# Optimization experiments

Measured on AMD Instinct MI355X. Metric: run time of the kernel, lower is better.

The kernel has to match this reference:

```python
import jax, jax.numpy as jnp
import numpy as np

N = 10000      # nodes per QA graph
E = 128000     # edges per QA graph
A = 5          # answers (multiple choice)
D = 300        # glove embedding dim
H = 8          # heads layer 1
C1 = 64        # per-head out channels layer 1 (concat -> 512)
HID = 512
NEG_SLOPE = 0.2
EPS = 1e-16


def gat_layer(x, edge_index, W, a_src, a_dst, bias, concat):
    # x: [N, Din]; edge_index: [2, E]; W: [Din, H*C]; a_src/a_dst: [H, C]
    Hh, C = a_src.shape
    h = (x @ W).reshape(N, Hh, C)                      # transformed node feats
    alpha_src = (h * a_src[None]).sum(-1)              # [N, H]
    alpha_dst = (h * a_dst[None]).sum(-1)              # [N, H]
    src, dst = edge_index[0], edge_index[1]
    e = jax.nn.leaky_relu(alpha_src[src] + alpha_dst[dst], NEG_SLOPE)  # [E, H]
    # edge softmax grouped by destination node
    m = jax.ops.segment_max(e, dst, num_segments=N)    # [N, H]
    ex = jnp.exp(e - m[dst])
    denom = jax.ops.segment_sum(ex, dst, num_segments=N)
    alpha = ex / (denom[dst] + EPS)                    # [E, H]
    msg = alpha[:, :, None] * h[src]                   # [E, H, C]
    out = jax.ops.segment_sum(msg, dst, num_segments=N)  # [N, H, C]
    out = out.reshape(N, Hh * C) if concat else out.mean(axis=1)
    return out + bias, alpha


def setup_inputs() -> dict:
    key = jax.random.key(0)
    ks = jax.random.split(key, 10)
    s = 0.05
    return {
        "x": jax.random.normal(ks[0], (A, N, D), jnp.float32),
        "edge_index": jax.random.randint(ks[1], (A, 2, E), 0, N, dtype=jnp.int32),
        "W1": jax.random.normal(ks[2], (D, H * C1), jnp.float32) * s,
        "att_src1": jax.random.normal(ks[3], (H, C1), jnp.float32) * s,
        "att_dst1": jax.random.normal(ks[4], (H, C1), jnp.float32) * s,
        "bias1": jnp.zeros((H * C1,), jnp.float32),
        "W2": jax.random.normal(ks[5], (HID, 1), jnp.float32) * s,
        "att_src2": jax.random.normal(ks[6], (1, 1), jnp.float32) * s,
        "att_dst2": jax.random.normal(ks[7], (1, 1), jnp.float32) * s,
        "bias2": jnp.zeros((1,), jnp.float32),
    }


def reference(x, edge_index, W1, att_src1, att_dst1, bias1, W2, att_src2, att_dst2, bias2):
    def per_answer(xa, ei):
        h1, _ = gat_layer(xa, ei, W1, att_src1, att_dst1, bias1, concat=True)
        h1 = jax.nn.relu(h1)
        h2, alpha = gat_layer(h1, ei, W2, att_src2, att_dst2, bias2, concat=False)
        proba = h2.mean()                                  # scalar (x.mean(dim=0))
        # aggregate_attention: attention[dst] += edge_weight (edge_additive)
        att = jax.ops.segment_sum(alpha[:, 0], ei[1], num_segments=N)
        return proba, att

    proba_vec, atts = jax.vmap(per_answer)(x, edge_index)  # [A], [A, N]
    sel = atts[jnp.argmax(proba_vec)]                      # attentions[argmax]
    return proba_vec, sel
```

## Files before the change

### kernel.cpp

```cpp
#include <hip/hip_runtime.h>
#include <hip/hip_bf16.h>
#include <math.h>

#define NN 10000
#define EE 128000
#define AA 5
#define DD 300
#define HH 8
#define CC 64
#define HC 512
#define MM (AA*NN)
#define KP 320
#define NT (KP / 32)
#define NBM ((MM + 63) / 64)
#define SCB 40
#define SCN 250

typedef __attribute__((ext_vector_type(8))) _Float16 f16x8;
typedef __attribute__((ext_vector_type(4))) float f32x4;
typedef __attribute__((ext_vector_type(2))) float f32x2;
typedef unsigned short ushort;
typedef unsigned char uchar;

__device__ __forceinline__ ushort f2bf(float f) {
    unsigned u = __float_as_uint(f);
    unsigned r = u + 0x7fffu + ((u >> 16) & 1u);
    return (ushort)(r >> 16);
}
__device__ __forceinline__ float bf2f(ushort h) {
    return __uint_as_float(((unsigned)h) << 16);
}
__device__ __forceinline__ float leaky_exp(float v) {
    v = v > 0.f ? v : 0.2f * v;
    return __expf(v);
}


__global__ void zero_cnt(int* cnt) {
    int i = blockIdx.x * 256 + threadIdx.x;
    if (i < AA * NN) cnt[i] = 0;
}

__global__ void count_edges(const int* __restrict__ ei, int* __restrict__ cnt) {
    int a = blockIdx.y;
    int e = blockIdx.x * 256 + threadIdx.x;
    if (e < EE) {
        int dst = ei[(size_t)a * 2 * EE + EE + e];
        atomicAdd(&cnt[a * NN + dst], 1);
    }
}


__global__ __launch_bounds__(256) void scan_bsum(const int* __restrict__ cnt,
                                                 int* __restrict__ bsum) {
    int a = blockIdx.y, b = blockIdx.x;
    int l = threadIdx.x;
    int v = (l < SCN) ? cnt[a * NN + b * SCN + l] : 0;
    #pragma unroll
    for (int o = 1; o < 64; o <<= 1) v += __shfl_xor(v, o);
    __shared__ int red[4];
    if ((l & 63) == 0) red[l >> 6] = v;
    __syncthreads();
    if (l == 0) bsum[a * SCB + b] = red[0] + red[1] + red[2] + red[3];
}

__global__ __launch_bounds__(64) void scan_bscan(const int* __restrict__ bsum,
                                                 int* __restrict__ boff,
                                                 int* __restrict__ offs) {
    int a = blockIdx.x;
    int l = threadIdx.x;
    int v = (l < SCB) ? bsum[a * SCB + l] : 0;
    int sc = v;
    #pragma unroll
    for (int o = 1; o < 64; o <<= 1) {
        int u = __shfl_up(sc, o);
        if (l >= o) sc += u;
    }
    if (l < SCB) boff[a * SCB + l] = sc - v;
    if (l == 63) offs[a * (NN + 1) + NN] = sc;
}

__global__ __launch_bounds__(256) void scan_final(const int* __restrict__ cnt,
                                                  const int* __restrict__ boff,
                                                  int* __restrict__ offs,
                                                  int* __restrict__ cursor) {
    int a = blockIdx.y, b = blockIdx.x;
    int l = threadIdx.x;
    int i = b * SCN + l;
    int v = (l < SCN) ? cnt[a * NN + i] : 0;
    int sc = v;
    int lane = l & 63, wv = l >> 6;
    #pragma unroll
    for (int o = 1; o < 64; o <<= 1) {
        int u = __shfl_up(sc, o);
        if (lane >= o) sc += u;
    }
    __shared__ int ws[4];
    if (lane == 63) ws[wv] = sc;
    __syncthreads();
    int woff = 0;
    #pragma unroll
    for (int w = 0; w < 4; ++w) woff += (w < wv) ? ws[w] : 0;
    if (l < SCN) {
        int o = boff[a * SCB + b] + woff + sc - v;
        offs[a * (NN + 1) + i] = o;
        cursor[a * (NN + 1) + i] = o;
    }
}

__global__ void scatter_edges(const int* __restrict__ ei, int* __restrict__ cursor,
                              int* __restrict__ csr_eid) {
    int a = blockIdx.y;
    int e = blockIdx.x * 256 + threadIdx.x;
    if (e < EE) {
        int dst = ei[(size_t)a * 2 * EE + EE + e];
        int pos = atomicAdd(&cursor[a * (NN + 1) + dst], 1);
        csr_eid[(size_t)a * EE + pos] = e;
    }
}


__global__ __launch_bounds__(256) void sort_src(const int* __restrict__ ei,
                                                const int* __restrict__ offs,
                                                int* __restrict__ csr_eid,
                                                int* __restrict__ csr_src,
                                                const float* __restrict__ asrc,
                                                const float* __restrict__ adst,
                                                float* __restrict__ w_csr) {
    int a = blockIdx.y;
    int wid = threadIdx.x >> 6, l = threadIdx.x & 63;
    int n = blockIdx.x * 4 + wid;
    if (n >= NN) return;
    const int* offsA = offs + a * (NN + 1);
    int beg = offsA[n], end = offsA[n + 1];
    int deg = end - beg;
    int* seg = csr_eid + (size_t)a * EE + beg;
    const int* srcrow = ei + (size_t)a * 2 * EE;
    const float* asrcA = asrc + (size_t)a * NN * HH;
    const float* adstA = adst + (size_t)a * NN * HH;
    float4 d0 = *(const float4*)(adstA + (size_t)n * HH);
    float4 d1 = *(const float4*)(adstA + (size_t)n * HH + 4);

    if (deg <= 64) {
        int v = (l < deg) ? seg[l] : 0x7fffffff;
        #pragma unroll
        for (int k = 2; k <= 64; k <<= 1)
            #pragma unroll
            for (int j = k >> 1; j > 0; j >>= 1) {
                int p = __shfl_xor(v, j);
                bool keepMin = (((l & k) == 0) == ((l & j) == 0));
                int mn = min(v, p), mx = max(v, p);
                v = keepMin ? mn : mx;
            }
        if (l < deg) {
            int s = srcrow[v];
            csr_src[(size_t)a * EE + beg + l] = s;
            float4 s0 = *(const float4*)(asrcA + (size_t)s * HH);
            float4 s1 = *(const float4*)(asrcA + (size_t)s * HH + 4);
            float4 w0, w1;
            w0.x = leaky_exp(s0.x + d0.x); w0.y = leaky_exp(s0.y + d0.y);
            w0.z = leaky_exp(s0.z + d0.z); w0.w = leaky_exp(s0.w + d0.w);
            w1.x = leaky_exp(s1.x + d1.x); w1.y = leaky_exp(s1.y + d1.y);
            w1.z = leaky_exp(s1.z + d1.z); w1.w = leaky_exp(s1.w + d1.w);
            float* wp = w_csr + ((size_t)a * EE + beg + l) * HH;
            *(float4*)(wp) = w0;
            *(float4*)(wp + 4) = w1;
        }
    } else {
        if (l == 0) {
            for (int i = 1; i < deg; ++i) {
                int key = seg[i];
                int j = i - 1;
                while (j >= 0 && seg[j] > key) { seg[j + 1] = seg[j]; --j; }
                seg[j + 1] = key;
            }
        }
        __builtin_amdgcn_wave_barrier();
        for (int i = l; i < deg; i += 64) {
            int s = srcrow[seg[i]];
            csr_src[(size_t)a * EE + beg + i] = s;
            float4 s0 = *(const float4*)(asrcA + (size_t)s * HH);
            float4 s1 = *(const float4*)(asrcA + (size_t)s * HH + 4);
            float4 w0, w1;
            w0.x = leaky_exp(s0.x + d0.x); w0.y = leaky_exp(s0.y + d0.y);
            w0.z = leaky_exp(s0.z + d0.z); w0.w = leaky_exp(s0.w + d0.w);
            w1.x = leaky_exp(s1.x + d1.x); w1.y = leaky_exp(s1.y + d1.y);
            w1.z = leaky_exp(s1.z + d1.z); w1.w = leaky_exp(s1.w + d1.w);
            float* wp = w_csr + ((size_t)a * EE + beg + i) * HH;
            *(float4*)(wp) = w0;
            *(float4*)(wp + 4) = w1;
        }
    }
}


__global__ __launch_bounds__(256) void pack_x(const float* __restrict__ X,
                                              ushort* __restrict__ Xp) {
    int gid = blockIdx.x * 256 + threadIdx.x;
    if (gid >= NBM * NT * 4 * 64) return;
    int l = gid & 63;
    int fr = (gid >> 6) & 3;
    int rest = gid >> 8;
    int ks = rest % NT;
    int bmi = rest / NT;
    int row = bmi * 64 + fr * 16 + (l & 15);
    int k = ks * 32 + (l >> 4) * 8;
    f16x8 o;
    if (row < MM && k + 8 <= DD) {
        float4 v0 = *(const float4*)(X + (size_t)row * DD + k);
        float4 v1 = *(const float4*)(X + (size_t)row * DD + k + 4);
        o[0] = (_Float16)v0.x; o[1] = (_Float16)v0.y;
        o[2] = (_Float16)v0.z; o[3] = (_Float16)v0.w;
        o[4] = (_Float16)v1.x; o[5] = (_Float16)v1.y;
        o[6] = (_Float16)v1.z; o[7] = (_Float16)v1.w;
    } else {
        #pragma unroll
        for (int j = 0; j < 8; ++j)
            o[j] = (row < MM && k + j < DD) ? (_Float16)X[(size_t)row * DD + k + j]
                                            : (_Float16)0.f;
    }
    *(f16x8*)(Xp + (size_t)gid * 8) = o;
}

__global__ __launch_bounds__(256) void pack_w(const float* __restrict__ W,
                                              ushort* __restrict__ Wp) {
    int gid = blockIdx.x * 256 + threadIdx.x;
    if (gid >= HH * NT * 4 * 64) return;
    int l = gid & 63;
    int fc = (gid >> 6) & 3;
    int rest = gid >> 8;
    int ks = rest % NT;
    int head = rest / NT;
    int col = head * 64 + fc * 16 + (l & 15);
    int k = ks * 32 + (l >> 4) * 8;
    f16x8 o;
    #pragma unroll
    for (int j = 0; j < 8; ++j)
        o[j] = (k + j < DD) ? (_Float16)W[(size_t)(k + j) * HC + col] : (_Float16)0.f;
    *(f16x8*)(Wp + (size_t)gid * 8) = o;
}


__global__ __launch_bounds__(256) void gemm_f16(const ushort* __restrict__ Xp,
                                                const ushort* __restrict__ Wp,
                                                const float* __restrict__ att_src1,
                                                const float* __restrict__ att_dst1,
                                                uchar* __restrict__ Hout,
                                                float* __restrict__ asrc,
                                                float* __restrict__ adst) {
    int wid = blockIdx.x * 4 + (threadIdx.x >> 6);
    int bmi = wid >> 3, head = wid & 7;
    if (bmi >= NBM) return;
    int bm = bmi * 64;
    int l = threadIdx.x & 63;
    int l16 = l & 15, kg = l >> 4;

    const ushort* Abase = Xp + (size_t)bmi * NT * 2048 + l * 8;
    const ushort* Bbase = Wp + (size_t)head * NT * 2048 + l * 8;

    f32x4 zz = {0.f, 0.f, 0.f, 0.f};
    f32x4 acc[4][4];
    #pragma unroll
    for (int i = 0; i < 4; ++i)
        #pragma unroll
        for (int j = 0; j < 4; ++j) acc[i][j] = zz;

    f16x8 aX[4], bX[4], aY[4], bY[4];
    #pragma unroll
    for (int f = 0; f < 4; ++f) {
        aX[f] = *(const f16x8*)(Abase + f * 512);
        bX[f] = *(const f16x8*)(Bbase + f * 512);
    }

    #pragma unroll
    for (int kk = 0; kk < NT; kk += 2) {
        if (kk + 1 < NT) {
            #pragma unroll
            for (int f = 0; f < 4; ++f) {
                aY[f] = *(const f16x8*)(Abase + (kk + 1) * 2048 + f * 512);
                bY[f] = *(const f16x8*)(Bbase + (kk + 1) * 2048 + f * 512);
            }
        }
        #pragma unroll
        for (int fr = 0; fr < 4; ++fr)
            #pragma unroll
            for (int fc = 0; fc < 4; ++fc)
                acc[fr][fc] = __builtin_amdgcn_mfma_f32_16x16x32_f16(aX[fr], bX[fc], acc[fr][fc], 0, 0, 0);
        if (kk + 2 < NT) {
            #pragma unroll
            for (int f = 0; f < 4; ++f) {
                aX[f] = *(const f16x8*)(Abase + (kk + 2) * 2048 + f * 512);
                bX[f] = *(const f16x8*)(Bbase + (kk + 2) * 2048 + f * 512);
            }
        }
        if (kk + 1 < NT) {
            #pragma unroll
            for (int fr = 0; fr < 4; ++fr)
                #pragma unroll
                for (int fc = 0; fc < 4; ++fc)
                    acc[fr][fc] = __builtin_amdgcn_mfma_f32_16x16x32_f16(aY[fr], bY[fc], acc[fr][fc], 0, 0, 0);
        }
    }

    float sv[4], dv[4];
    #pragma unroll
    for (int fc = 0; fc < 4; ++fc) {
        sv[fc] = att_src1[head * 64 + fc * 16 + l16];
        dv[fc] = att_dst1[head * 64 + fc * 16 + l16];
    }
    #pragma unroll
    for (int fr = 0; fr < 4; ++fr) {
        #pragma unroll
        for (int r = 0; r < 4; ++r) {
            int row = bm + fr * 16 + kg * 4 + r;
            bool ok = row < MM;
            float ps = 0.f, pd = 0.f;
            #pragma unroll
            for (int fc = 0; fc < 4; ++fc) {
                float val = acc[fr][fc][r];
                if (ok) {
                    int pk = __builtin_amdgcn_cvt_pk_fp8_f32(val, val, 0, false);
                    Hout[(size_t)row * HC + head * 64 + fc * 16 + l16] = (uchar)(pk & 0xff);
                }
                ps = fmaf(val, sv[fc], ps);
                pd = fmaf(val, dv[fc], pd);
            }
            #pragma unroll
            for (int o = 1; o < 16; o <<= 1) {
                ps += __shfl_xor(ps, o);
                pd += __shfl_xor(pd, o);
            }
            if (l16 == 0 && ok) {
                asrc[(size_t)row * HH + head] = ps;
                adst[(size_t)row * HH + head] = pd;
            }
        }
    }
}


__global__ __launch_bounds__(256) void layer1_agg(const uchar* __restrict__ h1,
                                                  const float* __restrict__ w_csr,
                                                  const int* __restrict__ offs,
                                                  const int* __restrict__ csr_src,
                                                  const float* __restrict__ bias1,
                                                  const float* __restrict__ W2,
                                                  float* __restrict__ h2) {
    int a = blockIdx.y;
    int wid = threadIdx.x >> 6, l = threadIdx.x & 63;
    int n = blockIdx.x * 4 + wid;
    int eg = l >> 3;
    int gh = l >> 3;

    const int* offsA = offs + a * (NN + 1);
    int beg = offsA[n], end = offsA[n + 1];
    int deg = end - beg;
    const int* srcs = csr_src + (size_t)a * EE + beg;
    const float* wA = w_csr + ((size_t)a * EE + beg) * HH;
    const uchar* h1A = h1 + (size_t)a * NN * HC;

    float denom = 0.f;
    float acc[8] = {};

    float w_cur = (eg < deg) ? wA[l] : 0.f;
    int s_cur = (eg < deg) ? srcs[eg] : 0;

    for (int c0 = 0; c0 < deg; c0 += 8) {
        float w_nxt = 0.f;
        int s_nxt = 0;
        if (c0 + 8 + eg < deg) {
            w_nxt = wA[(c0 + 8) * 8 + l];
            s_nxt = srcs[c0 + 8 + eg];
        }
        #pragma unroll
        for (int j = 0; j < 8; ++j) {
            if (c0 + j < deg) {
                float wj = __shfl(w_cur, j * 8 + gh);
                int sj = __shfl(s_cur, j * 8);
                uint2 hv = *(const uint2*)(h1A + (size_t)sj * HC + (l << 3));
                f32x2 p0 = __builtin_amdgcn_cvt_pk_f32_fp8((int)hv.x, false);
                f32x2 p1 = __builtin_amdgcn_cvt_pk_f32_fp8((int)hv.x, true);
                f32x2 p2 = __builtin_amdgcn_cvt_pk_f32_fp8((int)hv.y, false);
                f32x2 p3 = __builtin_amdgcn_cvt_pk_f32_fp8((int)hv.y, true);
                acc[0] = fmaf(wj, p0[0], acc[0]);
                acc[1] = fmaf(wj, p0[1], acc[1]);
                acc[2] = fmaf(wj, p1[0], acc[2]);
                acc[3] = fmaf(wj, p1[1], acc[3]);
                acc[4] = fmaf(wj, p2[0], acc[4]);
                acc[5] = fmaf(wj, p2[1], acc[5]);
                acc[6] = fmaf(wj, p3[0], acc[6]);
                acc[7] = fmaf(wj, p3[1], acc[7]);
            }
        }
        denom += w_cur;
        w_cur = w_nxt;
        s_cur = s_nxt;
    }
    #pragma unroll
    for (int o = 8; o < 64; o <<= 1) denom += __shfl_xor(denom, o);
    float dn = __shfl(denom, gh);
    float inv = 1.f / (dn + 1e-16f);

    int cb = l * 8;
    float4 b0 = *(const float4*)(bias1 + cb);
    float4 b1 = *(const float4*)(bias1 + cb + 4);
    float4 w0 = *(const float4*)(W2 + cb);
    float4 w1 = *(const float4*)(W2 + cb + 4);
    float bz[8] = {b0.x, b0.y, b0.z, b0.w, b1.x, b1.y, b1.z, b1.w};
    float wz[8] = {w0.x, w0.y, w0.z, w0.w, w1.x, w1.y, w1.z, w1.w};
    float p = 0.f;
    #pragma unroll
    for (int k = 0; k < 8; ++k) {
        float z = fmaf(acc[k], inv, bz[k]);
        z = z > 0.f ? z : 0.f;
        p = fmaf(z, wz[k], p);
    }
    #pragma unroll
    for (int o = 1; o < 64; o <<= 1) p += __shfl_xor(p, o);
    if (l == 0) h2[(size_t)a * NN + n] = p;
}


#define L2GRID 40

__global__ __launch_bounds__(256) void layer2_proba(const float* __restrict__ h2,
                                                    const int* __restrict__ offs,
                                                    const int* __restrict__ csr_src,
                                                    const float* __restrict__ att_src2,
                                                    const float* __restrict__ att_dst2,
                                                    const float* __restrict__ bias2,
                                                    float* __restrict__ partials) {
    int a = blockIdx.y;
    int n = blockIdx.x * 256 + threadIdx.x;
    float out2 = 0.f;
    if (n < NN) {
        const int* offsA = offs + a * (NN + 1);
        const int* srcs = csr_src + (size_t)a * EE;
        const float* h2A = h2 + (size_t)a * NN;
        float as2 = att_src2[0], ad2 = att_dst2[0];
        int beg = offsA[n], end = offsA[n + 1];
        float adn = h2A[n] * ad2;
        float denom = 0.f, accv = 0.f;
        for (int i = beg; i < end; ++i) {
            float hs = h2A[srcs[i]];
            float v = fmaf(hs, as2, adn);
            v = v > 0.f ? v : 0.2f * v;
            float w = __expf(v);
            denom += w;
            accv = fmaf(w, hs, accv);
        }
        out2 = accv / (denom + 1e-16f) + bias2[0];
    }
    __shared__ float red[256];
    red[threadIdx.x] = out2;
    __syncthreads();
    for (int s = 128; s > 0; s >>= 1) {
        if (threadIdx.x < s) red[threadIdx.x] += red[threadIdx.x + s];
        __syncthreads();
    }
    if (threadIdx.x == 0) partials[a * L2GRID + blockIdx.x] = red[0];
}

__global__ __launch_bounds__(256) void finalize_proba(const float* __restrict__ partials,
                                                      float* __restrict__ out,
                                                      int* __restrict__ best) {
    int tid = threadIdx.x;
    __shared__ float red[256];
    red[tid] = (tid < AA * L2GRID) ? partials[tid] : 0.f;
    __syncthreads();
    if (tid == 0) {
        float pv[AA];
        for (int a = 0; a < AA; ++a) {
            float s = 0.f;
            for (int i = 0; i < L2GRID; ++i) s += red[a * L2GRID + i];
            pv[a] = s / (float)NN;
            out[a] = pv[a];
        }
        int b = 0;
        for (int a = 1; a < AA; ++a)
            if (pv[a] > pv[b]) b = a;
        *best = b;
    }
}

__global__ void write_sel(const int* __restrict__ cnt, const int* __restrict__ best,
                          float* __restrict__ out) {
    int n = blockIdx.x * 256 + threadIdx.x;
    if (n < NN) out[AA + n] = (cnt[(*best) * NN + n] > 0) ? 1.0f : 0.0f;
}


extern "C" void kernel_launch(void* const* d_in, const int* in_sizes, int n_in,
                              void* d_out, int out_size, void* d_ws, size_t ws_size,
                              hipStream_t stream) {
    const float* x        = (const float*)d_in[0];
    const int*   ei       = (const int*)d_in[1];
    const float* W1       = (const float*)d_in[2];
    const float* att_src1 = (const float*)d_in[3];
    const float* att_dst1 = (const float*)d_in[4];
    const float* bias1    = (const float*)d_in[5];
    const float* W2       = (const float*)d_in[6];
    const float* att_src2 = (const float*)d_in[7];
    const float* att_dst2 = (const float*)d_in[8];
    const float* bias2    = (const float*)d_in[9];
    float* out = (float*)d_out;

    char* ws = (char*)d_ws;
    size_t off = 0;
    auto alloc = [&](size_t bytes) {
        size_t cur = off;
        off += (bytes + 255) & ~(size_t)255;
        return cur;
    };
    uchar*  h1      = (uchar*)(ws + alloc(sizeof(uchar) * (size_t)MM * HC));
    ushort* xp      = (ushort*)(ws + alloc(sizeof(ushort) * (size_t)NBM * NT * 2048));
    float*  asrc    = (float*)(ws + alloc(sizeof(float) * (size_t)MM * HH));
    float*  adst    = (float*)(ws + alloc(sizeof(float) * (size_t)MM * HH));
    float*  h2      = (float*)(ws + alloc(sizeof(float) * (size_t)MM));
    int*    cnt     = (int*)(ws + alloc(sizeof(int) * (size_t)AA * NN));
    int*    offs    = (int*)(ws + alloc(sizeof(int) * (size_t)AA * (NN + 1)));
    int*    cursor  = (int*)(ws + alloc(sizeof(int) * (size_t)AA * (NN + 1)));
    int*    bsum    = (int*)(ws + alloc(sizeof(int) * (size_t)AA * SCB));
    int*    boff    = (int*)(ws + alloc(sizeof(int) * (size_t)AA * SCB));
    int*    csr_eid = (int*)(ws + alloc(sizeof(int) * (size_t)AA * EE));
    int*    csr_src = (int*)(ws + alloc(sizeof(int) * (size_t)AA * EE));
    float*  w_csr   = (float*)(ws + alloc(sizeof(float) * (size_t)AA * EE * HH));
    float*  partials= (float*)(ws + alloc(sizeof(float) * AA * L2GRID));
    int*    best    = (int*)(ws + alloc(sizeof(int) * 16));
    ushort* wp      = (ushort*)(ws + alloc(sizeof(ushort) * (size_t)HH * NT * 2048));
    (void)ws_size; (void)in_sizes; (void)n_in; (void)out_size;

    pack_w<<<dim3((HH * NT * 256 + 255) / 256), dim3(256), 0, stream>>>(W1, wp);
    pack_x<<<dim3((NBM * NT * 256 + 255) / 256), dim3(256), 0, stream>>>(x, xp);

    zero_cnt<<<dim3((AA * NN + 255) / 256), dim3(256), 0, stream>>>(cnt);
    count_edges<<<dim3(EE / 256, AA), dim3(256), 0, stream>>>(ei, cnt);
    scan_bsum<<<dim3(SCB, AA), dim3(256), 0, stream>>>(cnt, bsum);
    scan_bscan<<<dim3(AA), dim3(64), 0, stream>>>(bsum, boff, offs);
    scan_final<<<dim3(SCB, AA), dim3(256), 0, stream>>>(cnt, boff, offs, cursor);
    scatter_edges<<<dim3(EE / 256, AA), dim3(256), 0, stream>>>(ei, cursor, csr_eid);

    gemm_f16<<<dim3((NBM * 8 + 3) / 4), dim3(256), 0, stream>>>(
        xp, wp, att_src1, att_dst1, h1, asrc, adst);

    sort_src<<<dim3(NN / 4, AA), dim3(256), 0, stream>>>(ei, offs, csr_eid, csr_src,
                                                         asrc, adst, w_csr);

    layer1_agg<<<dim3(NN / 4, AA), dim3(256), 0, stream>>>(h1, w_csr, offs, csr_src,
                                                           bias1, W2, h2);

    layer2_proba<<<dim3(L2GRID, AA), dim3(256), 0, stream>>>(h2, offs, csr_src,
                                                             att_src2, att_dst2, bias2,
                                                             partials);

    finalize_proba<<<dim3(1), dim3(256), 0, stream>>>(partials, out, best);
    write_sel<<<dim3((NN + 255) / 256), dim3(256), 0, stream>>>(cnt, best, out);
}
```

Baseline: 235.6 us.

## Compute two heads per wave in GEMM, simplify aggregation loads, memset counts

The GEMM now has each wave compute two heads for one 64-row block, so each A fragment feeds both heads' MFMAs and is loaded half as often. The accumulator count doubles, which raises register pressure and may lower occupancy. The layer-1 aggregation drops the shuffle-based prefetch of weights and sources and reads them directly per edge instead. The zeroing kernel is replaced with hipMemsetAsync.

```diff
diff --git a/kernel.cpp b/kernel.cpp
--- a/kernel.cpp
+++ b/kernel.cpp
@@ -35,11 +35,6 @@
     return __expf(v);
 }
 
-
-__global__ void zero_cnt(int* cnt) {
-    int i = blockIdx.x * 256 + threadIdx.x;
-    if (i < AA * NN) cnt[i] = 0;
-}
 
 __global__ void count_edges(const int* __restrict__ ei, int* __restrict__ cnt) {
     int a = blockIdx.y;
@@ -249,27 +244,29 @@
                                                 float* __restrict__ asrc,
                                                 float* __restrict__ adst) {
     int wid = blockIdx.x * 4 + (threadIdx.x >> 6);
-    int bmi = wid >> 3, head = wid & 7;
+    int bmi = wid >> 2, hp = wid & 3;
     if (bmi >= NBM) return;
     int bm = bmi * 64;
     int l = threadIdx.x & 63;
     int l16 = l & 15, kg = l >> 4;
 
     const ushort* Abase = Xp + (size_t)bmi * NT * 2048 + l * 8;
-    const ushort* Bbase = Wp + (size_t)head * NT * 2048 + l * 8;
+    const ushort* B0 = Wp + (size_t)(hp * 2) * NT * 2048 + l * 8;
+    const ushort* B1 = Wp + (size_t)(hp * 2 + 1) * NT * 2048 + l * 8;
 
     f32x4 zz = {0.f, 0.f, 0.f, 0.f};
-    f32x4 acc[4][4];
+    f32x4 acc0[4][4], acc1[4][4];
     #pragma unroll
     for (int i = 0; i < 4; ++i)
         #pragma unroll
-        for (int j = 0; j < 4; ++j) acc[i][j] = zz;
-
-    f16x8 aX[4], bX[4], aY[4], bY[4];
+        for (int j = 0; j < 4; ++j) { acc0[i][j] = zz; acc1[i][j] = zz; }
+
+    f16x8 aX[4], b0X[4], b1X[4], aY[4], b0Y[4], b1Y[4];
     #pragma unroll
     for (int f = 0; f < 4; ++f) {
-        aX[f] = *(const f16x8*)(Abase + f * 512);
-        bX[f] = *(const f16x8*)(Bbase + f * 512);
+        aX[f]  = *(const f16x8*)(Abase + f * 512);
+        b0X[f] = *(const f16x8*)(B0 + f * 512);
+        b1X[f] = *(const f16x8*)(B1 + f * 512);
     }
 
     #pragma unroll
@@ -277,62 +274,72 @@
         if (kk + 1 < NT) {
             #pragma unroll
             for (int f = 0; f < 4; ++f) {
-                aY[f] = *(const f16x8*)(Abase + (kk + 1) * 2048 + f * 512);
-                bY[f] = *(const f16x8*)(Bbase + (kk + 1) * 2048 + f * 512);
+                aY[f]  = *(const f16x8*)(Abase + (kk + 1) * 2048 + f * 512);
+                b0Y[f] = *(const f16x8*)(B0 + (kk + 1) * 2048 + f * 512);
+                b1Y[f] = *(const f16x8*)(B1 + (kk + 1) * 2048 + f * 512);
             }
         }
         #pragma unroll
         for (int fr = 0; fr < 4; ++fr)
             #pragma unroll
-            for (int fc = 0; fc < 4; ++fc)
-                acc[fr][fc] = __builtin_amdgcn_mfma_f32_16x16x32_f16(aX[fr], bX[fc], acc[fr][fc], 0, 0, 0);
+            for (int fc = 0; fc < 4; ++fc) {
+                acc0[fr][fc] = __builtin_amdgcn_mfma_f32_16x16x32_f16(aX[fr], b0X[fc], acc0[fr][fc], 0, 0, 0);
+                acc1[fr][fc] = __builtin_amdgcn_mfma_f32_16x16x32_f16(aX[fr], b1X[fc], acc1[fr][fc], 0, 0, 0);
+            }
         if (kk + 2 < NT) {
             #pragma unroll
             for (int f = 0; f < 4; ++f) {
-                aX[f] = *(const f16x8*)(Abase + (kk + 2) * 2048 + f * 512);
-                bX[f] = *(const f16x8*)(Bbase + (kk + 2) * 2048 + f * 512);
+                aX[f]  = *(const f16x8*)(Abase + (kk + 2) * 2048 + f * 512);
+                b0X[f] = *(const f16x8*)(B0 + (kk + 2) * 2048 + f * 512);
+                b1X[f] = *(const f16x8*)(B1 + (kk + 2) * 2048 + f * 512);
             }
         }
         if (kk + 1 < NT) {
             #pragma unroll
             for (int fr = 0; fr < 4; ++fr)
                 #pragma unroll
-                for (int fc = 0; fc < 4; ++fc)
-                    acc[fr][fc] = __builtin_amdgcn_mfma_f32_16x16x32_f16(aY[fr], bY[fc], acc[fr][fc], 0, 0, 0);
-        }
-    }
-
-    float sv[4], dv[4];
-    #pragma unroll
-    for (int fc = 0; fc < 4; ++fc) {
-        sv[fc] = att_src1[head * 64 + fc * 16 + l16];
-        dv[fc] = att_dst1[head * 64 + fc * 16 + l16];
-    }
-    #pragma unroll
-    for (int fr = 0; fr < 4; ++fr) {
-        #pragma unroll
-        for (int r = 0; r < 4; ++r) {
-            int row = bm + fr * 16 + kg * 4 + r;
-            bool ok = row < MM;
-            float ps = 0.f, pd = 0.f;
+                for (int fc = 0; fc < 4; ++fc) {
+                    acc0[fr][fc] = __builtin_amdgcn_mfma_f32_16x16x32_f16(aY[fr], b0Y[fc], acc0[fr][fc], 0, 0, 0);
+                    acc1[fr][fc] = __builtin_amdgcn_mfma_f32_16x16x32_f16(aY[fr], b1Y[fc], acc1[fr][fc], 0, 0, 0);
+                }
+        }
+    }
+
+    #pragma unroll
+    for (int hd = 0; hd < 2; ++hd) {
+        int head = hp * 2 + hd;
+        float sv[4], dv[4];
+        #pragma unroll
+        for (int fc = 0; fc < 4; ++fc) {
+            sv[fc] = att_src1[head * 64 + fc * 16 + l16];
+            dv[fc] = att_dst1[head * 64 + fc * 16 + l16];
+        }
+        #pragma unroll
+        for (int fr = 0; fr < 4; ++fr) {
             #pragma unroll
-            for (int fc = 0; fc < 4; ++fc) {
-                float val = acc[fr][fc][r];
-                if (ok) {
-                    int pk = __builtin_amdgcn_cvt_pk_fp8_f32(val, val, 0, false);
-                    Hout[(size_t)row * HC + head * 64 + fc * 16 + l16] = (uchar)(pk & 0xff);
+            for (int r = 0; r < 4; ++r) {
+                int row = bm + fr * 16 + kg * 4 + r;
+                bool ok = row < MM;
+                float ps = 0.f, pd = 0.f;
+                #pragma unroll
+                for (int fc = 0; fc < 4; ++fc) {
+                    float val = hd == 0 ? acc0[fr][fc][r] : acc1[fr][fc][r];
+                    if (ok) {
+                        int pk = __builtin_amdgcn_cvt_pk_fp8_f32(val, val, 0, false);
+                        Hout[(size_t)row * HC + head * 64 + fc * 16 + l16] = (uchar)(pk & 0xff);
+                    }
+                    ps = fmaf(val, sv[fc], ps);
+                    pd = fmaf(val, dv[fc], pd);
                 }
-                ps = fmaf(val, sv[fc], ps);
-                pd = fmaf(val, dv[fc], pd);
-            }
-            #pragma unroll
-            for (int o = 1; o < 16; o <<= 1) {
-                ps += __shfl_xor(ps, o);
-                pd += __shfl_xor(pd, o);
-            }
-            if (l16 == 0 && ok) {
-                asrc[(size_t)row * HH + head] = ps;
-                adst[(size_t)row * HH + head] = pd;
+                #pragma unroll
+                for (int o = 1; o < 16; o <<= 1) {
+                    ps += __shfl_xor(ps, o);
+                    pd += __shfl_xor(pd, o);
+                }
+                if (l16 == 0 && ok) {
+                    asrc[(size_t)row * HH + head] = ps;
+                    adst[(size_t)row * HH + head] = pd;
+                }
             }
         }
     }
@@ -349,7 +356,6 @@
     int a = blockIdx.y;
     int wid = threadIdx.x >> 6, l = threadIdx.x & 63;
     int n = blockIdx.x * 4 + wid;
-    int eg = l >> 3;
     int gh = l >> 3;
 
     const int* offsA = offs + a * (NN + 1);
@@ -362,21 +368,14 @@
     float denom = 0.f;
     float acc[8] = {};
 
-    float w_cur = (eg < deg) ? wA[l] : 0.f;
-    int s_cur = (eg < deg) ? srcs[eg] : 0;
-
     for (int c0 = 0; c0 < deg; c0 += 8) {
-        float w_nxt = 0.f;
-        int s_nxt = 0;
-        if (c0 + 8 + eg < deg) {
-            w_nxt = wA[(c0 + 8) * 8 + l];
-            s_nxt = srcs[c0 + 8 + eg];
-        }
+        float wv = (c0 + gh < deg) ? wA[c0 * 8 + l] : 0.f;
+        denom += wv;
         #pragma unroll
         for (int j = 0; j < 8; ++j) {
             if (c0 + j < deg) {
-                float wj = __shfl(w_cur, j * 8 + gh);
-                int sj = __shfl(s_cur, j * 8);
+                int sj = srcs[c0 + j];
+                float wj = wA[(c0 + j) * 8 + gh];
                 uint2 hv = *(const uint2*)(h1A + (size_t)sj * HC + (l << 3));
                 f32x2 p0 = __builtin_amdgcn_cvt_pk_f32_fp8((int)hv.x, false);
                 f32x2 p1 = __builtin_amdgcn_cvt_pk_f32_fp8((int)hv.x, true);
@@ -392,9 +391,6 @@
                 acc[7] = fmaf(wj, p3[1], acc[7]);
             }
         }
-        denom += w_cur;
-        w_cur = w_nxt;
-        s_cur = s_nxt;
     }
     #pragma unroll
     for (int o = 8; o < 64; o <<= 1) denom += __shfl_xor(denom, o);
@@ -533,14 +529,14 @@
     pack_w<<<dim3((HH * NT * 256 + 255) / 256), dim3(256), 0, stream>>>(W1, wp);
     pack_x<<<dim3((NBM * NT * 256 + 255) / 256), dim3(256), 0, stream>>>(x, xp);
 
-    zero_cnt<<<dim3((AA * NN + 255) / 256), dim3(256), 0, stream>>>(cnt);
+    hipMemsetAsync(cnt, 0, sizeof(int) * (size_t)AA * NN, stream);
     count_edges<<<dim3(EE / 256, AA), dim3(256), 0, stream>>>(ei, cnt);
     scan_bsum<<<dim3(SCB, AA), dim3(256), 0, stream>>>(cnt, bsum);
     scan_bscan<<<dim3(AA), dim3(64), 0, stream>>>(bsum, boff, offs);
     scan_final<<<dim3(SCB, AA), dim3(256), 0, stream>>>(cnt, boff, offs, cursor);
     scatter_edges<<<dim3(EE / 256, AA), dim3(256), 0, stream>>>(ei, cursor, csr_eid);
 
-    gemm_f16<<<dim3((NBM * 8 + 3) / 4), dim3(256), 0, stream>>>(
+    gemm_f16<<<dim3(NBM), dim3(256), 0, stream>>>(
         xp, wp, att_src1, att_dst1, h1, asrc, adst);
 
     sort_src<<<dim3(NN / 4, AA), dim3(256), 0, stream>>>(ei, offs, csr_eid, csr_src,
```

New measurement: 287.3 us. 1.22x slower.
